# Kernel tuning notes

Hardware: AMD Instinct MI355X
Metric: run time of the kernel (lower is better)

## Reference

```python
import jax, jax.numpy as jnp
import numpy as np

N, R, B, H, C, E = 4096, 8, 30, 64, 16, 131072


def setup_inputs() -> dict:
    key = jax.random.key(0)
    ks = jax.random.split(key, 11)
    s = 0.02  # small init scale for weights
    return {
        "x": jax.random.normal(ks[0], (N, N), jnp.float32),
        "edge_index": jax.random.randint(ks[1], (2, E), 0, N, jnp.int32),
        "edge_type": jax.random.randint(ks[2], (E,), 0, R, jnp.int32),
        "basis1": jax.random.normal(ks[3], (B, N, H), jnp.float32) * s,
        "att1": jax.random.normal(ks[4], (R, B), jnp.float32) * s,
        "root1": jax.random.normal(ks[5], (N, H), jnp.float32) * s,
        "bias1": jnp.zeros((H,), jnp.float32),
        "basis2": jax.random.normal(ks[6], (B, H, C), jnp.float32) * s,
        "att2": jax.random.normal(ks[7], (R, B), jnp.float32) * s,
        "root2": jax.random.normal(ks[8], (H, C), jnp.float32) * s,
        "bias2": jnp.zeros((C,), jnp.float32),
    }


def _rgcn_conv(x, src, dst, etype, deg_inv, basis, att, root, bias):
    # Basis-decomposed relation weights: W_r = sum_b att[r,b] * basis[b]
    W = jnp.einsum("rb,bio->rio", att, basis)            # [R, in, out]
    # Pre-transform every node by every relation weight (equivalent to
    # per-edge bmm(x_j, W[edge_type]) but avoids gathering [E, in] features).
    h = jnp.einsum("ni,rio->nro", x, W)                  # [N, R, out]
    msg = h[src, etype]                                  # [E, out] per-edge message
    agg = jax.ops.segment_sum(msg, dst, num_segments=N)  # scatter-add to dst
    agg = agg * deg_inv[:, None]                         # scatter-mean (aggr='mean')
    return agg + x @ root + bias                         # root/self transform + bias


def reference(x, edge_index, edge_type, basis1, att1, root1, bias1,
              basis2, att2, root2, bias2):
    src, dst = edge_index[0], edge_index[1]
    deg = jax.ops.segment_sum(jnp.ones((E,), jnp.float32), dst, num_segments=N)
    deg_inv = 1.0 / jnp.maximum(deg, 1.0)  # zero in-degree -> 0 output, as scatter_mean
    h = jax.nn.relu(_rgcn_conv(x, src, dst, edge_type, deg_inv,
                               basis1, att1, root1, bias1))
    out = _rgcn_conv(h, src, dst, edge_type, deg_inv,
                     basis2, att2, root2, bias2)
    return jax.nn.log_softmax(out, axis=1)
```

## Files before the change

kernel.cpp:

```cpp
#include <hip/hip_runtime.h>
#include <cstdint>

#define E_CNT 131072
#define N_CNT 4096

typedef short bf16x8 __attribute__((ext_vector_type(8)));
typedef float f32x4 __attribute__((ext_vector_type(4)));

__device__ __forceinline__ ushort f2bf(float f) {
  union { float f; unsigned u; } v; v.f = f;
  unsigned r = v.u + 0x7FFFu + ((v.u >> 16) & 1u);
  return (ushort)(r >> 16);
}
__device__ __forceinline__ float bf2f(ushort u) {
  union { unsigned u; float f; } v; v.u = ((unsigned)u) << 16;
  return v.f;
}

__global__ __launch_bounds__(256) void k_prep(const float4* __restrict__ x,
                                              ushort* __restrict__ xbf,
                                              const int* __restrict__ dstp,
                                              int* __restrict__ deg,
                                              const float* __restrict__ att1,
                                              const float* __restrict__ basis1,
                                              const float* __restrict__ root1,
                                              ushort* __restrict__ wt1) {
  __shared__ float sT[32 * 33];
  int bid = blockIdx.x, t = threadIdx.x;
  if (bid < 256) {
    int i0 = (bid >> 1) * 32, o0 = (bid & 1) * 32;
    int ol = t & 31, ir = t >> 5;
    float a[8][4] = {};
    for (int b = 0; b < 30; b += 2) {
      float v0[4], v1[4];
#pragma unroll
      for (int k = 0; k < 4; ++k) {
        size_t ofs = (size_t)(i0 + ir + k * 8) * 64 + o0 + ol;
        v0[k] = basis1[(size_t)b * 262144 + ofs];
        v1[k] = basis1[(size_t)(b + 1) * 262144 + ofs];
      }
#pragma unroll
      for (int r = 0; r < 8; ++r) {
        float w0 = att1[r * 30 + b], w1 = att1[r * 30 + b + 1];
#pragma unroll
        for (int k = 0; k < 4; ++k) a[r][k] += w0 * v0[k] + w1 * v1[k];
      }
    }
    for (int r = 0; r < 8; ++r) {
#pragma unroll
      for (int k = 0; k < 4; ++k) sT[ol * 33 + ir + k * 8] = a[r][k];
      __syncthreads();
#pragma unroll
      for (int k = 0; k < 4; ++k) {
        int orow = ir + k * 8, icol = ol;
        wt1[(size_t)(r * 64 + o0 + orow) * 4096 + i0 + icol] = f2bf(sT[orow * 33 + icol]);
      }
      __syncthreads();
    }
  } else if (bid < 384) {
    int bb = bid - 256;
    int i0 = bb * 32;
    int ol = t & 31, ir = t >> 5;
    for (int oh = 0; oh < 2; ++oh) {
      int o0 = oh * 32;
#pragma unroll
      for (int k = 0; k < 4; ++k)
        sT[ol * 33 + ir + k * 8] = root1[(size_t)(i0 + ir + k * 8) * 64 + o0 + ol];
      __syncthreads();
#pragma unroll
      for (int k = 0; k < 4; ++k) {
        int orow = ir + k * 8, icol = ol;
        wt1[(size_t)(512 + o0 + orow) * 4096 + i0 + icol] = f2bf(sT[orow * 33 + icol]);
      }
      __syncthreads();
    }
  } else if (bid < 896) {
    int e = (bid - 384) * 256 + t;
    atomicAdd(&deg[dstp[e]], 1);
  } else {
    int i = (bid - 896) * 256 + t;
    float4 v0 = x[i * 2], v1 = x[i * 2 + 1];
    ushort o[8];
    o[0] = f2bf(v0.x); o[1] = f2bf(v0.y); o[2] = f2bf(v0.z); o[3] = f2bf(v0.w);
    o[4] = f2bf(v1.x); o[5] = f2bf(v1.y); o[6] = f2bf(v1.z); o[7] = f2bf(v1.w);
    *(ulonglong2*)(xbf + (size_t)i * 8) = *(const ulonglong2*)o;
  }
}

__global__ __launch_bounds__(1024) void k_scan(const int* __restrict__ deg,
                                               int* __restrict__ rowptr,
                                               int* __restrict__ cursor,
                                               float* __restrict__ dinv) {
  __shared__ int part[1024];
  int t = threadIdx.x;
  int base = t * 4;
  int d0 = deg[base], d1 = deg[base + 1], d2 = deg[base + 2], d3 = deg[base + 3];
  int s = d0 + d1 + d2 + d3;
  part[t] = s;
  __syncthreads();
  for (int off = 1; off < 1024; off <<= 1) {
    int v = part[t];
    int u = (t >= off) ? part[t - off] : 0;
    __syncthreads();
    part[t] = v + u;
    __syncthreads();
  }
  int incl = part[t];
  int excl = incl - s;
  int p0 = excl, p1 = excl + d0, p2 = p1 + d1, p3 = p2 + d2;
  rowptr[base] = p0; rowptr[base + 1] = p1; rowptr[base + 2] = p2; rowptr[base + 3] = p3;
  cursor[base] = p0; cursor[base + 1] = p1; cursor[base + 2] = p2; cursor[base + 3] = p3;
  dinv[base]     = 1.0f / fmaxf((float)d0, 1.0f);
  dinv[base + 1] = 1.0f / fmaxf((float)d1, 1.0f);
  dinv[base + 2] = 1.0f / fmaxf((float)d2, 1.0f);
  dinv[base + 3] = 1.0f / fmaxf((float)d3, 1.0f);
  if (t == 1023) rowptr[4096] = incl;
}

__global__ __launch_bounds__(256) void k_mid(const int* __restrict__ srcp,
                                             const int* __restrict__ dstp,
                                             const int* __restrict__ et,
                                             int* __restrict__ cursor,
                                             int* __restrict__ spack,
                                             const float* __restrict__ att2,
                                             const float* __restrict__ basis2,
                                             const float* __restrict__ root2,
                                             float* __restrict__ w2e) {
  int bid = blockIdx.x, t = threadIdx.x;
  if (bid < 512) {
    int e = bid * 256 + t;
    int d = dstp[e];
    int pos = atomicAdd(&cursor[d], 1);
    spack[pos] = (srcp[e] << 3) | et[e];
  } else {
    int r = bid - 512;
    for (int q = t; q < 1024; q += 256) {
      float a = 0.f;
      if (r < 8) {
        for (int b = 0; b < 30; ++b) a += att2[r * 30 + b] * basis2[b * 1024 + q];
      } else {
        a = root2[q];
      }
      w2e[r * 1024 + q] = a;
    }
  }
}

__global__ __launch_bounds__(256, 6) void k_gemm1(const ushort* __restrict__ xbf,
                                                  const ushort* __restrict__ wt1,
                                                  float* __restrict__ c1p) {
  __shared__ __align__(16) ushort As[128 * 64];
  __shared__ __align__(16) ushort Bs[64 * 64];
  int bid = blockIdx.x;
  int swz = (bid & 7) * 144 + (bid >> 3);
  int kp = swz / 288, rem = swz % 288;
  int bm = rem / 9, bn = rem % 9;
  int m0 = bm * 128, n0 = bn * 64, kbase = kp * 1024;
  int tid = threadIdx.x;
  int lane = tid & 63, wid = tid >> 6;
  int wm = wid >> 1, wn = wid & 1;

  f32x4 acc[4][2] = {};

  for (int tt = 0; tt < 16; ++tt) {
    int k0 = kbase + tt * 64;
#pragma unroll
    for (int it = 0; it < 4; ++it) {
      int flat = it * 256 + tid;
      int row = flat >> 3, gg = flat & 7;
      int gcol = k0 + ((gg ^ (row & 7)) << 3);
      const ushort* g = xbf + (size_t)(m0 + row) * 4096 + gcol;
      ushort* l = &As[(it * 256 + wid * 64) * 8];
      __builtin_amdgcn_global_load_lds((const __attribute__((address_space(1))) void*)g,
                                       (__attribute__((address_space(3))) void*)l, 16, 0, 0);
    }
#pragma unroll
    for (int it = 0; it < 2; ++it) {
      int flat = it * 256 + tid;
      int row = flat >> 3, gg = flat & 7;
      int gcol = k0 + ((gg ^ (row & 7)) << 3);
      const ushort* g = wt1 + (size_t)(n0 + row) * 4096 + gcol;
      ushort* l = &Bs[(it * 256 + wid * 64) * 8];
      __builtin_amdgcn_global_load_lds((const __attribute__((address_space(1))) void*)g,
                                       (__attribute__((address_space(3))) void*)l, 16, 0, 0);
    }
    __syncthreads();
    int q = lane >> 4, sw = lane & 7, r16 = lane & 15;
#pragma unroll
    for (int ks = 0; ks < 2; ++ks) {
      int co = ((ks * 4 + q) ^ sw) << 3;
      bf16x8 b0 = *(const bf16x8*)&Bs[(wn * 32 + 0 * 16 + r16) * 64 + co];
      bf16x8 b1 = *(const bf16x8*)&Bs[(wn * 32 + 1 * 16 + r16) * 64 + co];
      bf16x8 a0 = *(const bf16x8*)&As[(wm * 64 + 0 * 16 + r16) * 64 + co];
      bf16x8 a1 = *(const bf16x8*)&As[(wm * 64 + 1 * 16 + r16) * 64 + co];
      bf16x8 a2 = *(const bf16x8*)&As[(wm * 64 + 2 * 16 + r16) * 64 + co];
      bf16x8 a3 = *(const bf16x8*)&As[(wm * 64 + 3 * 16 + r16) * 64 + co];
      __builtin_amdgcn_s_setprio(1);
      acc[0][0] = __builtin_amdgcn_mfma_f32_16x16x32_bf16(a0, b0, acc[0][0], 0, 0, 0);
      acc[0][1] = __builtin_amdgcn_mfma_f32_16x16x32_bf16(a0, b1, acc[0][1], 0, 0, 0);
      acc[1][0] = __builtin_amdgcn_mfma_f32_16x16x32_bf16(a1, b0, acc[1][0], 0, 0, 0);
      acc[1][1] = __builtin_amdgcn_mfma_f32_16x16x32_bf16(a1, b1, acc[1][1], 0, 0, 0);
      acc[2][0] = __builtin_amdgcn_mfma_f32_16x16x32_bf16(a2, b0, acc[2][0], 0, 0, 0);
      acc[2][1] = __builtin_amdgcn_mfma_f32_16x16x32_bf16(a2, b1, acc[2][1], 0, 0, 0);
      acc[3][0] = __builtin_amdgcn_mfma_f32_16x16x32_bf16(a3, b0, acc[3][0], 0, 0, 0);
      acc[3][1] = __builtin_amdgcn_mfma_f32_16x16x32_bf16(a3, b1, acc[3][1], 0, 0, 0);
      __builtin_amdgcn_s_setprio(0);
    }
    __syncthreads();
  }

  float* outp = c1p + (size_t)kp * 2359296;
  int cf = lane & 15, rf4 = (lane >> 4) * 4;
#pragma unroll
  for (int mi = 0; mi < 4; ++mi)
#pragma unroll
    for (int ni = 0; ni < 2; ++ni) {
      int gcol = n0 + wn * 32 + ni * 16 + cf;
#pragma unroll
      for (int j = 0; j < 4; ++j) {
        int grow = m0 + wm * 64 + mi * 16 + rf4 + j;
        outp[(size_t)grow * 576 + gcol] = acc[mi][ni][j];
      }
    }
}

__global__ __launch_bounds__(256) void k_reduce(const float4* __restrict__ p,
                                                ushort* __restrict__ c1bf) {
#pragma unroll
  for (int j = 0; j < 2; ++j) {
    int idx = blockIdx.x * 512 + j * 256 + threadIdx.x;
    float4 a = p[idx];
    float4 b = p[idx + 589824];
    float4 c = p[idx + 2 * 589824];
    float4 d = p[idx + 3 * 589824];
    float4 s;
    s.x = (a.x + b.x) + (c.x + d.x);
    s.y = (a.y + b.y) + (c.y + d.y);
    s.z = (a.z + b.z) + (c.z + d.z);
    s.w = (a.w + b.w) + (c.w + d.w);
    ushort4 o;
    o.x = f2bf(s.x); o.y = f2bf(s.y); o.z = f2bf(s.z); o.w = f2bf(s.w);
    *(ushort4*)(c1bf + (size_t)idx * 4) = o;
  }
}

__global__ __launch_bounds__(256) void k_agg1h2(const ushort* __restrict__ c1bf,
                                                const int* __restrict__ rowptr,
                                                const int* __restrict__ spack,
                                                const float* __restrict__ dinv,
                                                const float* __restrict__ bias1,
                                                const float* __restrict__ w2e,
                                                float* __restrict__ h2c) {
  __shared__ float sh[4][64];
  int g = threadIdx.x >> 6, t = threadIdx.x & 63;
  int n = blockIdx.x * 4 + g;
  int s0 = rowptr[n], s1 = rowptr[n + 1];
  float acc = 0.f;
  int e = s0;
  for (; e + 3 < s1; e += 4) {
    int p0 = spack[e], p1 = spack[e + 1], p2 = spack[e + 2], p3 = spack[e + 3];
    float v0 = bf2f(c1bf[(size_t)(p0 >> 3) * 576 + (p0 & 7) * 64 + t]);
    float v1 = bf2f(c1bf[(size_t)(p1 >> 3) * 576 + (p1 & 7) * 64 + t]);
    float v2 = bf2f(c1bf[(size_t)(p2 >> 3) * 576 + (p2 & 7) * 64 + t]);
    float v3 = bf2f(c1bf[(size_t)(p3 >> 3) * 576 + (p3 & 7) * 64 + t]);
    acc += (v0 + v1) + (v2 + v3);
  }
  for (; e < s1; ++e) {
    int p = spack[e];
    acc += bf2f(c1bf[(size_t)(p >> 3) * 576 + (p & 7) * 64 + t]);
  }
  float v = acc * dinv[n] + bf2f(c1bf[(size_t)n * 576 + 512 + t]) + bias1[t];
  sh[g][t] = fmaxf(v, 0.f);
  __syncthreads();
  float* o = h2c + (size_t)n * 144;
  for (int rc = t; rc < 144; rc += 64) {
    int r9 = rc >> 4, c = rc & 15;
    const float* w = w2e + r9 * 1024 + c;
    float a = 0.f;
#pragma unroll
    for (int hh = 0; hh < 64; ++hh) a += sh[g][hh] * w[hh * 16];
    o[rc] = a;
  }
}

__global__ __launch_bounds__(64) void k_agg2(const float* __restrict__ h2c,
                                             const int* __restrict__ rowptr,
                                             const int* __restrict__ spack,
                                             const float* __restrict__ dinv,
                                             const float* __restrict__ bias2,
                                             float* __restrict__ out) {
  __shared__ float red[64];
  int n = blockIdx.x, t = threadIdx.x;
  int c = t & 15, q = t >> 4;
  int s0 = rowptr[n], s1 = rowptr[n + 1];
  float acc = 0.f;
  for (int e = s0 + q; e < s1; e += 4) {
    int p = spack[e];
    acc += h2c[(size_t)(p >> 3) * 144 + (p & 7) * 16 + c];
  }
  red[t] = acc;
  __syncthreads();
  if (t < 16) {
    float sum = red[c] + red[16 + c] + red[32 + c] + red[48 + c];
    float v = sum * dinv[n] + h2c[(size_t)n * 144 + 128 + c] + bias2[c];
    float m = v;
#pragma unroll
    for (int off = 1; off < 16; off <<= 1) m = fmaxf(m, __shfl_xor(m, off, 64));
    float ex = expf(v - m);
    float s = ex;
#pragma unroll
    for (int off = 1; off < 16; off <<= 1) s += __shfl_xor(s, off, 64);
    out[n * 16 + c] = v - m - logf(s);
  }
}

extern "C" void kernel_launch(void* const* d_in, const int* in_sizes, int n_in,
                              void* d_out, int out_size, void* d_ws, size_t ws_size,
                              hipStream_t stream) {
  const float* x      = (const float*)d_in[0];
  const int*   ei     = (const int*)d_in[1];
  const int*   et     = (const int*)d_in[2];
  const float* basis1 = (const float*)d_in[3];
  const float* att1   = (const float*)d_in[4];
  const float* root1  = (const float*)d_in[5];
  const float* bias1  = (const float*)d_in[6];
  const float* basis2 = (const float*)d_in[7];
  const float* att2   = (const float*)d_in[8];
  const float* root2  = (const float*)d_in[9];
  const float* bias2  = (const float*)d_in[10];
  float* out = (float*)d_out;

  char* ws = (char*)d_ws;
  size_t off = 0;
  auto alloc = [&](size_t bytes) {
    void* p = ws + off;
    off = (off + bytes + 255) & ~(size_t)255;
    return p;
  };
  ushort* xbf  = (ushort*)alloc((size_t)N_CNT * N_CNT * 2);
  ushort* wt1  = (ushort*)alloc((size_t)576 * 4096 * 2);
  float*  c1p  = (float*)alloc((size_t)4 * N_CNT * 576 * 4);
  ushort* c1bf = (ushort*)alloc((size_t)N_CNT * 576 * 2);
  float*  w2e  = (float*)alloc((size_t)9 * 64 * 16 * 4);
  float*  h2c  = (float*)alloc((size_t)N_CNT * 144 * 4);
  int*    deg    = (int*)alloc(4096 * 4);
  float*  dinv   = (float*)alloc(4096 * 4);
  int*    rowptr = (int*)alloc(4097 * 4);
  int*    cursor = (int*)alloc(4096 * 4);
  int*    spack  = (int*)alloc((size_t)E_CNT * 4);

  const int* srcp = ei;
  const int* dstp = ei + E_CNT;

  hipMemsetAsync(deg, 0, 4096 * 4, stream);
  k_prep<<<9088, 256, 0, stream>>>((const float4*)x, xbf, dstp, deg,
                                   att1, basis1, root1, wt1);
  k_scan<<<1, 1024, 0, stream>>>(deg, rowptr, cursor, dinv);
  k_mid<<<521, 256, 0, stream>>>(srcp, dstp, et, cursor, spack,
                                 att2, basis2, root2, w2e);
  k_gemm1<<<1152, 256, 0, stream>>>(xbf, wt1, c1p);
  k_reduce<<<1152, 256, 0, stream>>>((const float4*)c1p, c1bf);
  k_agg1h2<<<1024, 256, 0, stream>>>(c1bf, rowptr, spack, dinv, bias1, w2e, h2c);
  k_agg2<<<4096, 64, 0, stream>>>(h2c, rowptr, spack, dinv, bias2, out);
}
```

Measured before the change: 134.5 us.

## Widen GEMM N-tile, use 8-way split-K with atomic accumulation, drop reduce kernel

The first GEMM now uses 128x192 tiles with an 8-way K split. Partial sums are accumulated directly into an fp32 output with atomicAdd, so the separate partial-buffer write and reduce/bf16-convert kernel are removed. The aggregation kernel then reads fp32 instead of bf16. The prep kernel is split into a conversion/degree kernel and a weight-combine kernel. This saves the partial-buffer traffic and one launch, but adds a memset, atomic contention, and twice-as-large gathers in aggregation.

```diff
diff --git a/kernel.cpp b/kernel.cpp
--- a/kernel.cpp
+++ b/kernel.cpp
@@ -12,19 +12,11 @@
   unsigned r = v.u + 0x7FFFu + ((v.u >> 16) & 1u);
   return (ushort)(r >> 16);
 }
-__device__ __forceinline__ float bf2f(ushort u) {
-  union { unsigned u; float f; } v; v.u = ((unsigned)u) << 16;
-  return v.f;
-}
-
-__global__ __launch_bounds__(256) void k_prep(const float4* __restrict__ x,
-                                              ushort* __restrict__ xbf,
-                                              const int* __restrict__ dstp,
-                                              int* __restrict__ deg,
-                                              const float* __restrict__ att1,
-                                              const float* __restrict__ basis1,
-                                              const float* __restrict__ root1,
-                                              ushort* __restrict__ wt1) {
+
+__global__ __launch_bounds__(256) void k_combine(const float* __restrict__ att1,
+                                                 const float* __restrict__ basis1,
+                                                 const float* __restrict__ root1,
+                                                 ushort* __restrict__ wt1) {
   __shared__ float sT[32 * 33];
   int bid = blockIdx.x, t = threadIdx.x;
   if (bid < 256) {
@@ -57,7 +49,7 @@
       }
       __syncthreads();
     }
-  } else if (bid < 384) {
+  } else {
     int bb = bid - 256;
     int i0 = bb * 32;
     int ol = t & 31, ir = t >> 5;
@@ -74,16 +66,24 @@
       }
       __syncthreads();
     }
-  } else if (bid < 896) {
-    int e = (bid - 384) * 256 + t;
-    atomicAdd(&deg[dstp[e]], 1);
-  } else {
-    int i = (bid - 896) * 256 + t;
+  }
+}
+
+__global__ __launch_bounds__(256) void k_cvt(const float4* __restrict__ x,
+                                             ushort* __restrict__ xbf,
+                                             const int* __restrict__ dstp,
+                                             int* __restrict__ deg) {
+  int bid = blockIdx.x, t = threadIdx.x;
+  if (bid < 8192) {
+    int i = bid * 256 + t;
     float4 v0 = x[i * 2], v1 = x[i * 2 + 1];
     ushort o[8];
     o[0] = f2bf(v0.x); o[1] = f2bf(v0.y); o[2] = f2bf(v0.z); o[3] = f2bf(v0.w);
     o[4] = f2bf(v1.x); o[5] = f2bf(v1.y); o[6] = f2bf(v1.z); o[7] = f2bf(v1.w);
     *(ulonglong2*)(xbf + (size_t)i * 8) = *(const ulonglong2*)o;
+  } else {
+    int e = (bid - 8192) * 256 + t;
+    atomicAdd(&deg[dstp[e]], 1);
   }
 }
 
@@ -146,23 +146,22 @@
   }
 }
 
-__global__ __launch_bounds__(256, 6) void k_gemm1(const ushort* __restrict__ xbf,
+__global__ __launch_bounds__(256, 3) void k_gemm1(const ushort* __restrict__ xbf,
                                                   const ushort* __restrict__ wt1,
-                                                  float* __restrict__ c1p) {
+                                                  float* __restrict__ c1) {
   __shared__ __align__(16) ushort As[128 * 64];
-  __shared__ __align__(16) ushort Bs[64 * 64];
+  __shared__ __align__(16) ushort Bs[192 * 64];
   int bid = blockIdx.x;
-  int swz = (bid & 7) * 144 + (bid >> 3);
-  int kp = swz / 288, rem = swz % 288;
-  int bm = rem / 9, bn = rem % 9;
-  int m0 = bm * 128, n0 = bn * 64, kbase = kp * 1024;
+  int kp = bid & 7, rem = bid >> 3;
+  int bm = rem / 3, bn = rem % 3;
+  int m0 = bm * 128, n0 = bn * 192, kbase = kp * 512;
   int tid = threadIdx.x;
   int lane = tid & 63, wid = tid >> 6;
   int wm = wid >> 1, wn = wid & 1;
 
-  f32x4 acc[4][2] = {};
-
-  for (int tt = 0; tt < 16; ++tt) {
+  f32x4 acc[4][6] = {};
+
+  for (int tt = 0; tt < 8; ++tt) {
     int k0 = kbase + tt * 64;
 #pragma unroll
     for (int it = 0; it < 4; ++it) {
@@ -175,7 +174,7 @@
                                        (__attribute__((address_space(3))) void*)l, 16, 0, 0);
     }
 #pragma unroll
-    for (int it = 0; it < 2; ++it) {
+    for (int it = 0; it < 6; ++it) {
       int flat = it * 256 + tid;
       int row = flat >> 3, gg = flat & 7;
       int gcol = k0 + ((gg ^ (row & 7)) << 3);
@@ -189,62 +188,39 @@
 #pragma unroll
     for (int ks = 0; ks < 2; ++ks) {
       int co = ((ks * 4 + q) ^ sw) << 3;
-      bf16x8 b0 = *(const bf16x8*)&Bs[(wn * 32 + 0 * 16 + r16) * 64 + co];
-      bf16x8 b1 = *(const bf16x8*)&Bs[(wn * 32 + 1 * 16 + r16) * 64 + co];
-      bf16x8 a0 = *(const bf16x8*)&As[(wm * 64 + 0 * 16 + r16) * 64 + co];
-      bf16x8 a1 = *(const bf16x8*)&As[(wm * 64 + 1 * 16 + r16) * 64 + co];
-      bf16x8 a2 = *(const bf16x8*)&As[(wm * 64 + 2 * 16 + r16) * 64 + co];
-      bf16x8 a3 = *(const bf16x8*)&As[(wm * 64 + 3 * 16 + r16) * 64 + co];
+      bf16x8 b[6], a[4];
+#pragma unroll
+      for (int ni = 0; ni < 6; ++ni)
+        b[ni] = *(const bf16x8*)&Bs[(wn * 96 + ni * 16 + r16) * 64 + co];
+#pragma unroll
+      for (int mi = 0; mi < 4; ++mi)
+        a[mi] = *(const bf16x8*)&As[(wm * 64 + mi * 16 + r16) * 64 + co];
       __builtin_amdgcn_s_setprio(1);
-      acc[0][0] = __builtin_amdgcn_mfma_f32_16x16x32_bf16(a0, b0, acc[0][0], 0, 0, 0);
-      acc[0][1] = __builtin_amdgcn_mfma_f32_16x16x32_bf16(a0, b1, acc[0][1], 0, 0, 0);
-      acc[1][0] = __builtin_amdgcn_mfma_f32_16x16x32_bf16(a1, b0, acc[1][0], 0, 0, 0);
-      acc[1][1] = __builtin_amdgcn_mfma_f32_16x16x32_bf16(a1, b1, acc[1][1], 0, 0, 0);
-      acc[2][0] = __builtin_amdgcn_mfma_f32_16x16x32_bf16(a2, b0, acc[2][0], 0, 0, 0);
-      acc[2][1] = __builtin_amdgcn_mfma_f32_16x16x32_bf16(a2, b1, acc[2][1], 0, 0, 0);
-      acc[3][0] = __builtin_amdgcn_mfma_f32_16x16x32_bf16(a3, b0, acc[3][0], 0, 0, 0);
-      acc[3][1] = __builtin_amdgcn_mfma_f32_16x16x32_bf16(a3, b1, acc[3][1], 0, 0, 0);
+#pragma unroll
+      for (int mi = 0; mi < 4; ++mi)
+#pragma unroll
+        for (int ni = 0; ni < 6; ++ni)
+          acc[mi][ni] = __builtin_amdgcn_mfma_f32_16x16x32_bf16(a[mi], b[ni], acc[mi][ni], 0, 0, 0);
       __builtin_amdgcn_s_setprio(0);
     }
     __syncthreads();
   }
 
-  float* outp = c1p + (size_t)kp * 2359296;
   int cf = lane & 15, rf4 = (lane >> 4) * 4;
 #pragma unroll
   for (int mi = 0; mi < 4; ++mi)
 #pragma unroll
-    for (int ni = 0; ni < 2; ++ni) {
-      int gcol = n0 + wn * 32 + ni * 16 + cf;
+    for (int ni = 0; ni < 6; ++ni) {
+      int gcol = n0 + wn * 96 + ni * 16 + cf;
 #pragma unroll
       for (int j = 0; j < 4; ++j) {
         int grow = m0 + wm * 64 + mi * 16 + rf4 + j;
-        outp[(size_t)grow * 576 + gcol] = acc[mi][ni][j];
-      }
-    }
-}
-
-__global__ __launch_bounds__(256) void k_reduce(const float4* __restrict__ p,
-                                                ushort* __restrict__ c1bf) {
-#pragma unroll
-  for (int j = 0; j < 2; ++j) {
-    int idx = blockIdx.x * 512 + j * 256 + threadIdx.x;
-    float4 a = p[idx];
-    float4 b = p[idx + 589824];
-    float4 c = p[idx + 2 * 589824];
-    float4 d = p[idx + 3 * 589824];
-    float4 s;
-    s.x = (a.x + b.x) + (c.x + d.x);
-    s.y = (a.y + b.y) + (c.y + d.y);
-    s.z = (a.z + b.z) + (c.z + d.z);
-    s.w = (a.w + b.w) + (c.w + d.w);
-    ushort4 o;
-    o.x = f2bf(s.x); o.y = f2bf(s.y); o.z = f2bf(s.z); o.w = f2bf(s.w);
-    *(ushort4*)(c1bf + (size_t)idx * 4) = o;
-  }
-}
-
-__global__ __launch_bounds__(256) void k_agg1h2(const ushort* __restrict__ c1bf,
+        atomicAdd(&c1[(size_t)grow * 576 + gcol], acc[mi][ni][j]);
+      }
+    }
+}
+
+__global__ __launch_bounds__(256) void k_agg1h2(const float* __restrict__ c1,
                                                 const int* __restrict__ rowptr,
                                                 const int* __restrict__ spack,
                                                 const float* __restrict__ dinv,
@@ -259,17 +235,17 @@
   int e = s0;
   for (; e + 3 < s1; e += 4) {
     int p0 = spack[e], p1 = spack[e + 1], p2 = spack[e + 2], p3 = spack[e + 3];
-    float v0 = bf2f(c1bf[(size_t)(p0 >> 3) * 576 + (p0 & 7) * 64 + t]);
-    float v1 = bf2f(c1bf[(size_t)(p1 >> 3) * 576 + (p1 & 7) * 64 + t]);
-    float v2 = bf2f(c1bf[(size_t)(p2 >> 3) * 576 + (p2 & 7) * 64 + t]);
-    float v3 = bf2f(c1bf[(size_t)(p3 >> 3) * 576 + (p3 & 7) * 64 + t]);
+    float v0 = c1[(size_t)(p0 >> 3) * 576 + (p0 & 7) * 64 + t];
+    float v1 = c1[(size_t)(p1 >> 3) * 576 + (p1 & 7) * 64 + t];
+    float v2 = c1[(size_t)(p2 >> 3) * 576 + (p2 & 7) * 64 + t];
+    float v3 = c1[(size_t)(p3 >> 3) * 576 + (p3 & 7) * 64 + t];
     acc += (v0 + v1) + (v2 + v3);
   }
   for (; e < s1; ++e) {
     int p = spack[e];
-    acc += bf2f(c1bf[(size_t)(p >> 3) * 576 + (p & 7) * 64 + t]);
-  }
-  float v = acc * dinv[n] + bf2f(c1bf[(size_t)n * 576 + 512 + t]) + bias1[t];
+    acc += c1[(size_t)(p >> 3) * 576 + (p & 7) * 64 + t];
+  }
+  float v = acc * dinv[n] + c1[(size_t)n * 576 + 512 + t] + bias1[t];
   sh[g][t] = fmaxf(v, 0.f);
   __syncthreads();
   float* o = h2c + (size_t)n * 144;
@@ -339,8 +315,7 @@
   };
   ushort* xbf  = (ushort*)alloc((size_t)N_CNT * N_CNT * 2);
   ushort* wt1  = (ushort*)alloc((size_t)576 * 4096 * 2);
-  float*  c1p  = (float*)alloc((size_t)4 * N_CNT * 576 * 4);
-  ushort* c1bf = (ushort*)alloc((size_t)N_CNT * 576 * 2);
+  float*  c1   = (float*)alloc((size_t)N_CNT * 576 * 4);
   float*  w2e  = (float*)alloc((size_t)9 * 64 * 16 * 4);
   float*  h2c  = (float*)alloc((size_t)N_CNT * 144 * 4);
   int*    deg    = (int*)alloc(4096 * 4);
@@ -353,13 +328,13 @@
   const int* dstp = ei + E_CNT;
 
   hipMemsetAsync(deg, 0, 4096 * 4, stream);
-  k_prep<<<9088, 256, 0, stream>>>((const float4*)x, xbf, dstp, deg,
-                                   att1, basis1, root1, wt1);
+  hipMemsetAsync(c1, 0, (size_t)N_CNT * 576 * 4, stream);
+  k_cvt<<<8704, 256, 0, stream>>>((const float4*)x, xbf, dstp, deg);
+  k_combine<<<384, 256, 0, stream>>>(att1, basis1, root1, wt1);
   k_scan<<<1, 1024, 0, stream>>>(deg, rowptr, cursor, dinv);
   k_mid<<<521, 256, 0, stream>>>(srcp, dstp, et, cursor, spack,
                                  att2, basis2, root2, w2e);
-  k_gemm1<<<1152, 256, 0, stream>>>(xbf, wt1, c1p);
-  k_reduce<<<1152, 256, 0, stream>>>((const float4*)c1p, c1bf);
-  k_agg1h2<<<1024, 256, 0, stream>>>(c1bf, rowptr, spack, dinv, bias1, w2e, h2c);
+  k_gemm1<<<768, 256, 0, stream>>>(xbf, wt1, c1);
+  k_agg1h2<<<1024, 256, 0, stream>>>(c1, rowptr, spack, dinv, bias1, w2e, h2c);
   k_agg2<<<4096, 64, 0, stream>>>(h2c, rowptr, spack, dinv, bias2, out);
 }
```

New measurement: 167.9 us. 24.9% more time.
